# Kernel tuning notes

Hardware: AMD Instinct MI355X
Metric: run time of the kernel (lower is better)

Reference implementation:

```python
import jax, jax.numpy as jnp
import numpy as np

B, N, C = 4, 2048, 1024
H = 16
D = C // H
FF = 4096
EPS = 1e-6


def _layernorm(x, g, b):
    mu = jnp.mean(x, axis=-1, keepdims=True)
    var = jnp.mean(jnp.square(x - mu), axis=-1, keepdims=True)
    return (x - mu) * jax.lax.rsqrt(var + EPS) * g + b


def setup_inputs() -> dict:
    key = jax.random.key(0)
    ks = jax.random.split(key, 8)
    s = 0.02
    x = jax.random.normal(ks[0], (B, N, C), dtype=jnp.float32)
    mask = jnp.tril(jnp.ones((N, N), dtype=bool))[None, None]  # causal [1,1,N,N]
    return {
        "x": x,
        "mask": mask,
        "qkv_w": jax.random.normal(ks[1], (3 * C, C), jnp.float32) * s,
        "qkv_b": jnp.zeros((3 * C,), jnp.float32),
        "proj_w": jax.random.normal(ks[2], (C, C), jnp.float32) * s,
        "proj_b": jnp.zeros((C,), jnp.float32),
        "ln1_g": jnp.ones((C,), jnp.float32),
        "ln1_b": jnp.zeros((C,), jnp.float32),
        "ln2_g": jnp.ones((C,), jnp.float32),
        "ln2_b": jnp.zeros((C,), jnp.float32),
        "w1": jax.random.normal(ks[3], (FF, C), jnp.float32) * s,
        "w2": jax.random.normal(ks[4], (C, FF), jnp.float32) * s,
        "w3": jax.random.normal(ks[5], (FF, C), jnp.float32) * s,
    }


def reference(x, mask, qkv_w, qkv_b, proj_w, proj_b, ln1_g, ln1_b, ln2_g, ln2_b, w1, w2, w3):
    # --- attention sub-block (pre-norm) ---
    h = _layernorm(x, ln1_g, ln1_b)
    qkv = h @ qkv_w.T + qkv_b                      # [B,N,3C]
    qkv = qkv.reshape(B, N, 3, H, D).transpose(2, 0, 3, 1, 4)  # [3,B,H,N,D]
    q, k, v = qkv[0], qkv[1], qkv[2]
    scale = D ** -0.5
    attn = jnp.einsum("bhnd,bhmd->bhnm", q, k) * scale
    attn = jnp.where(mask, attn, -jnp.inf)
    attn = jax.nn.softmax(attn, axis=-1)
    o = jnp.einsum("bhnm,bhmd->bhnd", attn, v)
    o = o.transpose(0, 2, 1, 3).reshape(B, N, C)
    o = o @ proj_w.T + proj_b
    x = x + o  # dropout is identity in eval mode
    # --- SwiGLU MLP sub-block (pre-norm) ---
    h = _layernorm(x, ln2_g, ln2_b)
    m = (jax.nn.silu(h @ w1.T) * (h @ w3.T)) @ w2.T
    return x + m
```

## Files before the change

### kernel.cpp

```cpp
#include <hip/hip_runtime.h>
#include <hip/hip_bf16.h>
#include <stdint.h>

#define NB   4
#define NSEQ 2048
#define NC   1024
#define NH   16
#define ND   64
#define NFF  4096
#define NM   (NB*NSEQ)

typedef __attribute__((ext_vector_type(8))) short short8v;
typedef __attribute__((ext_vector_type(4))) short short4v;
typedef __attribute__((ext_vector_type(4))) float f32x4;

#define GPTR(p) ((const __attribute__((address_space(1))) void*)(p))
#define LPTR(p) ((__attribute__((address_space(3))) void*)(p))

__device__ __forceinline__ short f2bf(float f){
  unsigned u = __builtin_bit_cast(unsigned, f);
  u += 0x7fffu + ((u >> 16) & 1u);
  return (short)(u >> 16);
}
__device__ __forceinline__ float bf2f(short h){
  unsigned u = ((unsigned)(unsigned short)h) << 16;
  return __builtin_bit_cast(float, u);
}
__device__ __forceinline__ f32x4 mfma16x32(short8v a, short8v b, f32x4 c){
  return __builtin_amdgcn_mfma_f32_16x16x32_bf16(a, b, c, 0, 0, 0);
}
__device__ __forceinline__ f32x4 mfma16x16(short4v a, short4v b, f32x4 c){
  return __builtin_amdgcn_mfma_f32_16x16x16bf16_1k(a, b, c, 0, 0, 0);
}
__device__ __forceinline__ short4v pack4bf(f32x4 v){
  __hip_bfloat162 a = __float22bfloat162_rn(float2{v[0], v[1]});
  __hip_bfloat162 b = __float22bfloat162_rn(float2{v[2], v[3]});
  short4v r;
  __builtin_memcpy(&r, &a, 4);
  __builtin_memcpy(((char*)&r) + 4, &b, 4);
  return r;
}

__global__ __launch_bounds__(256) void cvt_kernel(const float* __restrict__ w,
                                                  short* __restrict__ o, int n){
  int i = (blockIdx.x * 256 + threadIdx.x) * 4;
  if (i >= n) return;
  float4 v = *(const float4*)(w + i);
  short4v r = { f2bf(v.x), f2bf(v.y), f2bf(v.z), f2bf(v.w) };
  *(short4v*)(o + i) = r;
}

__global__ __launch_bounds__(256) void ln_kernel(const float* __restrict__ x,
                                                 const float* __restrict__ g,
                                                 const float* __restrict__ bta,
                                                 short* __restrict__ out){
  int row = blockIdx.x;
  int tid = threadIdx.x;
  int lane = tid & 63, w = tid >> 6;
  const float4* xr = (const float4*)(x + (size_t)row * NC);
  float4 v = xr[tid];
  float s1 = v.x + v.y + v.z + v.w;
  float s2 = v.x*v.x + v.y*v.y + v.z*v.z + v.w*v.w;
  #pragma unroll
  for (int off = 32; off; off >>= 1){
    s1 += __shfl_xor(s1, off);
    s2 += __shfl_xor(s2, off);
  }
  __shared__ float red[8];
  if (lane == 0){ red[w] = s1; red[4 + w] = s2; }
  __syncthreads();
  s1 = red[0] + red[1] + red[2] + red[3];
  s2 = red[4] + red[5] + red[6] + red[7];
  float mean = s1 * (1.0f / NC);
  float var  = s2 * (1.0f / NC) - mean * mean;
  float inv  = rsqrtf(var + 1e-6f);
  float4 gv = ((const float4*)g)[tid];
  float4 bv = ((const float4*)bta)[tid];
  short4v o = { f2bf((v.x - mean) * inv * gv.x + bv.x),
                f2bf((v.y - mean) * inv * gv.y + bv.y),
                f2bf((v.z - mean) * inv * gv.z + bv.z),
                f2bf((v.w - mean) * inv * gv.w + bv.w) };
  *(short4v*)(out + (size_t)row * NC + tid * 4) = o;
}

template<bool HAS_BIAS, bool HAS_RES, bool OUT_BF16, bool QKV_V>
__global__ __launch_bounds__(256, 3) void gemm_bt(const short* __restrict__ A,
                                                  const short* __restrict__ Bm,
                                                  const float* __restrict__ bias,
                                                  const float* __restrict__ res,
                                                  void* __restrict__ outp,
                                                  short* __restrict__ vt,
                                                  int Nc, int K){
  __shared__ short Al[128 * 64];
  __shared__ short Bl[128 * 64];
  int tid = threadIdx.x;
  int gx = gridDim.x, nwg = gx * gridDim.y;
  int wg = blockIdx.y * gx + blockIdx.x;
  int swz = (wg & 7) * (nwg >> 3) + (wg >> 3);
  int m0 = (swz / gx) * 128, n0 = (swz % gx) * 128;
  const short* Ag = A + (size_t)m0 * K;
  const short* Bg = Bm + (size_t)n0 * K;
  int lane = tid & 63, wid = tid >> 6;
  int wm = (wid >> 1) * 64, wn = (wid & 1) * 64;
  int qd = lane >> 4, l15 = lane & 15;

  f32x4 acc[4][4] = {};

  for (int k0 = 0; k0 < K; k0 += 64){
    __syncthreads();
    #pragma unroll
    for (int i = 0; i < 4; i++){
      int cg = (wid * 4 + i) * 64 + lane;
      int r  = cg >> 3, c = cg & 7;
      int sc = (c ^ (r & 7)) << 3;
      __builtin_amdgcn_global_load_lds(GPTR(Ag + (size_t)r * K + k0 + sc),
                                       LPTR(&Al[cg * 8]), 16, 0, 0);
      __builtin_amdgcn_global_load_lds(GPTR(Bg + (size_t)r * K + k0 + sc),
                                       LPTR(&Bl[cg * 8]), 16, 0, 0);
    }
    __syncthreads();
    #pragma unroll
    for (int kk = 0; kk < 2; kk++){
      short8v a[4], b[4];
      #pragma unroll
      for (int t = 0; t < 4; t++){
        int r = wm + t * 16 + l15;
        a[t] = *(const short8v*)&Al[r * 64 + (((kk * 4 + qd) ^ (r & 7)) << 3)];
      }
      #pragma unroll
      for (int t = 0; t < 4; t++){
        int r = wn + t * 16 + l15;
        b[t] = *(const short8v*)&Bl[r * 64 + (((kk * 4 + qd) ^ (r & 7)) << 3)];
      }
      #pragma unroll
      for (int i = 0; i < 4; i++)
        #pragma unroll
        for (int j = 0; j < 4; j++)
          acc[i][j] = mfma16x32(a[i], b[j], acc[i][j]);
    }
  }

  #pragma unroll
  for (int ti = 0; ti < 4; ti++){
    #pragma unroll
    for (int tj = 0; tj < 4; tj++){
      int col = n0 + wn + tj * 16 + l15;
      float bv = HAS_BIAS ? bias[col] : 0.0f;
      #pragma unroll
      for (int r = 0; r < 4; r++){
        int row = m0 + wm + ti * 16 + qd * 4 + r;
        float v = acc[ti][tj][r] + bv;
        if (QKV_V && col >= 2048){
          int hh = (col - 2048) >> 6, dd = col & 63;
          int bb = row >> 11, nn = row & 2047;
          vt[(((size_t)(bb * 16 + hh) * 64 + dd) << 11) + nn] = f2bf(v);
        } else {
          size_t idx = (size_t)row * Nc + col;
          if (HAS_RES) v += res[idx];
          if (OUT_BF16) ((short*)outp)[idx] = f2bf(v);
          else          ((float*)outp)[idx] = v;
        }
      }
    }
  }
}

__global__ __launch_bounds__(256, 2) void gemm_ff13(const short* __restrict__ A,
                                                    const short* __restrict__ B1m,
                                                    const short* __restrict__ B3m,
                                                    short* __restrict__ outp){
  __shared__ short Al [128 * 64];
  __shared__ short B1l[128 * 64];
  __shared__ short B3l[128 * 64];
  int tid = threadIdx.x;
  int gx = gridDim.x;
  int wg = blockIdx.y * gx + blockIdx.x;
  int xcd = wg & 7, idx = wg >> 3;
  int npx = gx >> 3;
  int n0 = (xcd * npx + idx % npx) * 128;
  int m0 = (idx / npx) * 128;
  const short* Ag  = A   + (size_t)m0 * NC;
  const short* B1g = B1m + (size_t)n0 * NC;
  const short* B3g = B3m + (size_t)n0 * NC;
  int lane = tid & 63, wid = tid >> 6;
  int wm = (wid >> 1) * 64, wn = (wid & 1) * 64;
  int qd = lane >> 4, l15 = lane & 15;

  f32x4 acc1[4][4] = {}, acc3[4][4] = {};

  for (int k0 = 0; k0 < NC; k0 += 64){
    __syncthreads();
    #pragma unroll
    for (int i = 0; i < 4; i++){
      int cg = (wid * 4 + i) * 64 + lane;
      int r  = cg >> 3, c = cg & 7;
      int sc = (c ^ (r & 7)) << 3;
      __builtin_amdgcn_global_load_lds(GPTR(Ag + (size_t)r * NC + k0 + sc),
                                       LPTR(&Al[cg * 8]), 16, 0, 0);
      __builtin_amdgcn_global_load_lds(GPTR(B1g + (size_t)r * NC + k0 + sc),
                                       LPTR(&B1l[cg * 8]), 16, 0, 0);
      __builtin_amdgcn_global_load_lds(GPTR(B3g + (size_t)r * NC + k0 + sc),
                                       LPTR(&B3l[cg * 8]), 16, 0, 0);
    }
    __syncthreads();
    #pragma unroll
    for (int kk = 0; kk < 2; kk++){
      short8v a[4], b1[4], b3[4];
      #pragma unroll
      for (int t = 0; t < 4; t++){
        int r = wm + t * 16 + l15;
        a[t] = *(const short8v*)&Al[r * 64 + (((kk * 4 + qd) ^ (r & 7)) << 3)];
      }
      #pragma unroll
      for (int t = 0; t < 4; t++){
        int r = wn + t * 16 + l15;
        int co = ((kk * 4 + qd) ^ (r & 7)) << 3;
        b1[t] = *(const short8v*)&B1l[r * 64 + co];
        b3[t] = *(const short8v*)&B3l[r * 64 + co];
      }
      #pragma unroll
      for (int i = 0; i < 4; i++)
        #pragma unroll
        for (int j = 0; j < 4; j++){
          acc1[i][j] = mfma16x32(a[i], b1[j], acc1[i][j]);
          acc3[i][j] = mfma16x32(a[i], b3[j], acc3[i][j]);
        }
    }
  }

  #pragma unroll
  for (int ti = 0; ti < 4; ti++){
    #pragma unroll
    for (int tj = 0; tj < 4; tj++){
      int col = n0 + wn + tj * 16 + l15;
      #pragma unroll
      for (int r = 0; r < 4; r++){
        int row = m0 + wm + ti * 16 + qd * 4 + r;
        float v1 = acc1[ti][tj][r];
        float v3 = acc3[ti][tj][r];
        float s = v1 / (1.0f + __expf(-v1)) * v3;
        outp[(size_t)row * NFF + col] = f2bf(s);
      }
    }
  }
}

__global__ __launch_bounds__(256) void attn_kernel(const short* __restrict__ qkvb,
                                                   const short* __restrict__ vt,
                                                   short* __restrict__ outb){
  const float QSCALE = 0.125f * 1.44269504f;
  int bh = blockIdx.x;
  int qb = 15 - blockIdx.y;
  int b = bh >> 4, h = bh & 15;
  int tid = threadIdx.x;
  int lane = tid & 63, wid = tid >> 6;
  int qd = lane >> 4, l15 = lane & 15;
  int qs = qb * 128 + wid * 32;

  const short* qbase = qkvb + (size_t)b * NSEQ * 3072 + h * 64;
  const short* kbase = qbase + 1024;
  const short* vtb   = vt + ((size_t)bh << 17);

  __shared__ short Kl[2][64 * 64];
  __shared__ short Vl[2][64 * 64];

  short8v qf[2][2];
  #pragma unroll
  for (int g = 0; g < 2; g++)
    #pragma unroll
    for (int kc = 0; kc < 2; kc++){
      short8v q = *(const short8v*)(qbase + (size_t)(qs + g * 16 + l15) * 3072
                                    + kc * 32 + qd * 8);
      short8v r;
      #pragma unroll
      for (int j = 0; j < 8; j++) r[j] = f2bf(bf2f(q[j]) * QSCALE);
      qf[g][kc] = r;
    }

  float l_i[2] = { 0.f, 0.f };
  f32x4 o[2][4];
  #pragma unroll
  for (int g = 0; g < 2; g++)
    #pragma unroll
    for (int t = 0; t < 4; t++)
      o[g][t] = (f32x4){0.f, 0.f, 0.f, 0.f};

  int nkt_blk = 2 * qb + 2;
  int itmax   = (qs + 31) >> 6;

  auto STAGE = [&](int bufi, int k0){
    #pragma unroll
    for (int i = 0; i < 2; i++){
      int cg = (wid * 2 + i) * 64 + lane;
      int r  = cg >> 3, c = cg & 7;
      int sc = (c ^ (r & 7)) << 3;
      __builtin_amdgcn_global_load_lds(GPTR(kbase + (size_t)(k0 + r) * 3072 + sc),
                                       LPTR(&Kl[bufi][cg * 8]), 16, 0, 0);
      __builtin_amdgcn_global_load_lds(GPTR(vtb + ((size_t)r << 11) + k0 + sc),
                                       LPTR(&Vl[bufi][cg * 8]), 16, 0, 0);
    }
  };

  STAGE(0, 0);
  __syncthreads();
  int cur = 0;

  for (int it = 0; it < nkt_blk; ++it){
    if (it + 1 < nkt_blk) STAGE(cur ^ 1, (it + 1) * 64);

    if (it <= itmax){
      int k0 = it * 64;
      short8v kf[4][2];
      #pragma unroll
      for (int kt = 0; kt < 4; kt++)
        #pragma unroll
        for (int kc = 0; kc < 2; kc++){
          int r = kt * 16 + l15;
          kf[kt][kc] = *(const short8v*)
              &Kl[cur][r * 64 + (((kc * 4 + qd) ^ (r & 7)) << 3)];
        }
      short4v vf[4][4];
      #pragma unroll
      for (int t = 0; t < 4; t++)
        #pragma unroll
        for (int ks = 0; ks < 4; ks++){
          int r = t * 16 + l15;
          vf[t][ks] = *(const short4v*)
              &Vl[cur][r * 64 + (((ks * 2 + (qd >> 1)) ^ (r & 7)) << 3)
                       + ((qd & 1) << 2)];
        }

      f32x4 s[2][4];
      #pragma unroll
      for (int g = 0; g < 2; g++)
        #pragma unroll
        for (int kt = 0; kt < 4; kt++){
          f32x4 z = (f32x4){0.f, 0.f, 0.f, 0.f};
          z = mfma16x32(kf[kt][0], qf[g][0], z);
          s[g][kt] = mfma16x32(kf[kt][1], qf[g][1], z);
        }

      if (it == itmax){
        #pragma unroll
        for (int g = 0; g < 2; g++){
          int qg = qs + g * 16 + l15;
          #pragma unroll
          for (int kt = 0; kt < 4; kt++)
            #pragma unroll
            for (int r = 0; r < 4; r++){
              int kg = k0 + kt * 16 + qd * 4 + r;
              s[g][kt][r] = (kg <= qg) ? s[g][kt][r] : -1e30f;
            }
        }
      }

      short4v pb[2][4];
      #pragma unroll
      for (int g = 0; g < 2; g++){
        #pragma unroll
        for (int kt = 0; kt < 4; kt++){
          f32x4 p;
          #pragma unroll
          for (int r = 0; r < 4; r++){
            float pv = exp2f(fminf(s[g][kt][r], 24.0f));
            p[r] = pv;
            l_i[g] += pv;
          }
          pb[g][kt] = pack4bf(p);
        }
      }

      #pragma unroll
      for (int g = 0; g < 2; g++)
        #pragma unroll
        for (int t = 0; t < 4; t++)
          #pragma unroll
          for (int ks = 0; ks < 4; ks++)
            o[g][t] = mfma16x16(vf[t][ks], pb[g][ks], o[g][t]);
    }

    __syncthreads();
    cur ^= 1;
  }

  #pragma unroll
  for (int g = 0; g < 2; g++){
    float l = l_i[g];
    l += __shfl_xor(l, 16);
    l += __shfl_xor(l, 32);
    float inv_l = 1.0f / l;
    int q = qs + g * 16 + l15;
    size_t rowbase = ((size_t)(b * NSEQ + q)) * NC + h * 64;
    #pragma unroll
    for (int t = 0; t < 4; t++){
      f32x4 v = { o[g][t][0] * inv_l, o[g][t][1] * inv_l,
                  o[g][t][2] * inv_l, o[g][t][3] * inv_l };
      *(short4v*)(outb + rowbase + t * 16 + qd * 4) = pack4bf(v);
    }
  }
}

extern "C" void kernel_launch(void* const* d_in, const int* in_sizes, int n_in,
                              void* d_out, int out_size, void* d_ws, size_t ws_size,
                              hipStream_t stream){
  const float* x      = (const float*)d_in[0];
  const float* qkv_w  = (const float*)d_in[2];
  const float* qkv_b  = (const float*)d_in[3];
  const float* proj_w = (const float*)d_in[4];
  const float* proj_b = (const float*)d_in[5];
  const float* ln1_g  = (const float*)d_in[6];
  const float* ln1_b  = (const float*)d_in[7];
  const float* ln2_g  = (const float*)d_in[8];
  const float* ln2_b  = (const float*)d_in[9];
  const float* w1     = (const float*)d_in[10];
  const float* w2     = (const float*)d_in[11];
  const float* w3     = (const float*)d_in[12];
  float* out = (float*)d_out;

  short* wqkv  = (short*)d_ws;
  short* wproj = wqkv  + (size_t)3072 * 1024;
  short* w1b   = wproj + (size_t)1024 * 1024;
  short* w3b   = w1b   + (size_t)4096 * 1024;
  short* w2b   = w3b   + (size_t)4096 * 1024;
  short* hb    = w2b   + (size_t)4096 * 1024;
  short* qkvb  = hb    + (size_t)NM * NC;
  short* attnb = qkvb  + (size_t)NM * 3072;
  short* ff3b  = attnb + (size_t)NM * NC;
  float* x1    = (float*)(ff3b + (size_t)NM * NFF);
  short* ff1b  = qkvb;
  short* vtb   = ff3b;

  cvt_kernel<<<3072 * 1024 / 1024, 256, 0, stream>>>(qkv_w, wqkv, 3072 * 1024);
  cvt_kernel<<<1024, 256, 0, stream>>>(proj_w, wproj, 1024 * 1024);
  cvt_kernel<<<4096, 256, 0, stream>>>(w1, w1b, 4096 * 1024);
  cvt_kernel<<<4096, 256, 0, stream>>>(w3, w3b, 4096 * 1024);
  cvt_kernel<<<4096, 256, 0, stream>>>(w2, w2b, 4096 * 1024);

  ln_kernel<<<NM, 256, 0, stream>>>(x, ln1_g, ln1_b, hb);
  gemm_bt<true, false, true, true><<<dim3(3072 / 128, NM / 128), 256, 0, stream>>>(
      hb, wqkv, qkv_b, nullptr, qkvb, vtb, 3072, 1024);
  attn_kernel<<<dim3(NB * NH, NSEQ / 128), 256, 0, stream>>>(qkvb, vtb, attnb);
  gemm_bt<true, true, false, false><<<dim3(1024 / 128, NM / 128), 256, 0, stream>>>(
      attnb, wproj, proj_b, x, x1, nullptr, 1024, 1024);
  ln_kernel<<<NM, 256, 0, stream>>>(x1, ln2_g, ln2_b, hb);
  gemm_ff13<<<dim3(4096 / 128, NM / 128), 256, 0, stream>>>(hb, w1b, w3b, ff1b);
  gemm_bt<false, true, false, false><<<dim3(1024 / 128, NM / 128), 256, 0, stream>>>(
      ff1b, w2b, nullptr, x1, out, nullptr, 1024, 4096);
}
```

Baseline: 554.1 us.

## Pipeline GEMMs with triple-buffered LDS and 256x128 tiles on 8 waves

Replaces the synchronous load-then-compute GEMM loops with a three-stage LDS ring. Tiles for k-step t+2 are prefetched via global_load_lds while MFMAs run on step t, with explicit vmcnt waits and raw barriers instead of __syncthreads. Workgroups grow to 512 threads covering 256x128 output tiles, and the FF13 kernel switches to a 32-wide K step with a new swizzle. This aims to hide global-load latency and raise data reuse per tile, at the cost of more LDS per block, lower occupancy and fragile hand-counted waitcnt logic.

```diff
diff --git a/kernel.cpp b/kernel.cpp
--- a/kernel.cpp
+++ b/kernel.cpp
@@ -84,60 +84,92 @@
 }
 
 template<bool HAS_BIAS, bool HAS_RES, bool OUT_BF16, bool QKV_V>
-__global__ __launch_bounds__(256, 3) void gemm_bt(const short* __restrict__ A,
-                                                  const short* __restrict__ Bm,
-                                                  const float* __restrict__ bias,
-                                                  const float* __restrict__ res,
-                                                  void* __restrict__ outp,
-                                                  short* __restrict__ vt,
-                                                  int Nc, int K){
-  __shared__ short Al[128 * 64];
-  __shared__ short Bl[128 * 64];
+__global__ __launch_bounds__(512) void gemm8p(const short* __restrict__ A,
+                                              const short* __restrict__ Bm,
+                                              const float* __restrict__ bias,
+                                              const float* __restrict__ res,
+                                              void* __restrict__ outp,
+                                              short* __restrict__ vt,
+                                              int Nc, int K){
+  __shared__ short lds[3][(256 + 128) * 64];
   int tid = threadIdx.x;
   int gx = gridDim.x, nwg = gx * gridDim.y;
   int wg = blockIdx.y * gx + blockIdx.x;
   int swz = (wg & 7) * (nwg >> 3) + (wg >> 3);
-  int m0 = (swz / gx) * 128, n0 = (swz % gx) * 128;
+  int m0 = (swz / gx) * 256, n0 = (swz % gx) * 128;
   const short* Ag = A + (size_t)m0 * K;
   const short* Bg = Bm + (size_t)n0 * K;
   int lane = tid & 63, wid = tid >> 6;
   int wm = (wid >> 1) * 64, wn = (wid & 1) * 64;
   int qd = lane >> 4, l15 = lane & 15;
 
+  auto STAGE_A = [&](short* buf, const short* src, int i){
+    int cg = i * 512 + tid;
+    int r = cg >> 3, c = cg & 7;
+    __builtin_amdgcn_global_load_lds(GPTR(src + (size_t)r * K + ((c ^ (r & 7)) << 3)),
+                                     LPTR(buf + cg * 8), 16, 0, 0);
+  };
+  auto STAGE_B = [&](short* buf, const short* src, int i){
+    int cg = i * 512 + tid;
+    int r = cg >> 3, c = cg & 7;
+    __builtin_amdgcn_global_load_lds(GPTR(src + (size_t)r * K + ((c ^ (r & 7)) << 3)),
+                                     LPTR(buf + 256 * 64 + cg * 8), 16, 0, 0);
+  };
+
+  short* b0 = &lds[0][0];
+  short* b1 = &lds[1][0];
+  short* b2 = &lds[2][0];
+
+  int nt = K >> 6;
+  #pragma unroll
+  for (int i = 0; i < 4; i++) STAGE_A(b0, Ag, i);
+  #pragma unroll
+  for (int i = 0; i < 2; i++) STAGE_B(b0, Bg, i);
+  #pragma unroll
+  for (int i = 0; i < 4; i++) STAGE_A(b1, Ag + 64, i);
+  #pragma unroll
+  for (int i = 0; i < 2; i++) STAGE_B(b1, Bg + 64, i);
+  asm volatile("s_waitcnt vmcnt(6)" ::: "memory");
+  __builtin_amdgcn_s_barrier();
+
   f32x4 acc[4][4] = {};
 
-  for (int k0 = 0; k0 < K; k0 += 64){
-    __syncthreads();
-    #pragma unroll
-    for (int i = 0; i < 4; i++){
-      int cg = (wid * 4 + i) * 64 + lane;
-      int r  = cg >> 3, c = cg & 7;
-      int sc = (c ^ (r & 7)) << 3;
-      __builtin_amdgcn_global_load_lds(GPTR(Ag + (size_t)r * K + k0 + sc),
-                                       LPTR(&Al[cg * 8]), 16, 0, 0);
-      __builtin_amdgcn_global_load_lds(GPTR(Bg + (size_t)r * K + k0 + sc),
-                                       LPTR(&Bl[cg * 8]), 16, 0, 0);
-    }
-    __syncthreads();
-    #pragma unroll
-    for (int kk = 0; kk < 2; kk++){
+  for (int t = 0; t < nt; ++t){
+    bool pf = (t + 2) < nt;
+    const short* As = Ag + (size_t)(t + 2) * 64;
+    const short* Bs = Bg + (size_t)(t + 2) * 64;
+    #pragma unroll
+    for (int p = 0; p < 2; p++){
       short8v a[4], b[4];
       #pragma unroll
-      for (int t = 0; t < 4; t++){
-        int r = wm + t * 16 + l15;
-        a[t] = *(const short8v*)&Al[r * 64 + (((kk * 4 + qd) ^ (r & 7)) << 3)];
-      }
-      #pragma unroll
-      for (int t = 0; t < 4; t++){
-        int r = wn + t * 16 + l15;
-        b[t] = *(const short8v*)&Bl[r * 64 + (((kk * 4 + qd) ^ (r & 7)) << 3)];
-      }
+      for (int u = 0; u < 4; u++){
+        int r = wm + u * 16 + l15;
+        a[u] = *(const short8v*)&b0[r * 64 + (((p * 4 + qd) ^ (r & 7)) << 3)];
+      }
+      #pragma unroll
+      for (int u = 0; u < 4; u++){
+        int r = wn + u * 16 + l15;
+        b[u] = *(const short8v*)&b0[256 * 64 + r * 64 + (((p * 4 + qd) ^ (r & 7)) << 3)];
+      }
+      if (pf){
+        if (p == 0){ STAGE_A(b2, As, 0); STAGE_A(b2, As, 1); STAGE_B(b2, Bs, 0); }
+        else       { STAGE_A(b2, As, 2); STAGE_A(b2, As, 3); STAGE_B(b2, Bs, 1); }
+      }
+      __builtin_amdgcn_s_barrier();
+      __builtin_amdgcn_s_setprio(1);
       #pragma unroll
       for (int i = 0; i < 4; i++)
         #pragma unroll
         for (int j = 0; j < 4; j++)
           acc[i][j] = mfma16x32(a[i], b[j], acc[i][j]);
-    }
+      __builtin_amdgcn_s_setprio(0);
+      if (p == 1){
+        if (pf)                asm volatile("s_waitcnt vmcnt(6)" ::: "memory");
+        else if (t + 1 < nt)   asm volatile("s_waitcnt vmcnt(0)" ::: "memory");
+      }
+      __builtin_amdgcn_s_barrier();
+    }
+    short* tmp = b0; b0 = b1; b1 = b2; b2 = tmp;
   }
 
   #pragma unroll
@@ -165,20 +197,19 @@
   }
 }
 
-__global__ __launch_bounds__(256, 2) void gemm_ff13(const short* __restrict__ A,
-                                                    const short* __restrict__ B1m,
-                                                    const short* __restrict__ B3m,
-                                                    short* __restrict__ outp){
-  __shared__ short Al [128 * 64];
-  __shared__ short B1l[128 * 64];
-  __shared__ short B3l[128 * 64];
+__global__ __launch_bounds__(512) void gemm_ff13(const short* __restrict__ A,
+                                                 const short* __restrict__ B1m,
+                                                 const short* __restrict__ B3m,
+                                                 short* __restrict__ outp){
+  __shared__ short lds[3][(256 + 128 + 128) * 32];
+  const int AOFF = 256 * 32, B3OFF = 256 * 32 + 128 * 32;
   int tid = threadIdx.x;
   int gx = gridDim.x;
   int wg = blockIdx.y * gx + blockIdx.x;
   int xcd = wg & 7, idx = wg >> 3;
   int npx = gx >> 3;
   int n0 = (xcd * npx + idx % npx) * 128;
-  int m0 = (idx / npx) * 128;
+  int m0 = (idx / npx) * 256;
   const short* Ag  = A   + (size_t)m0 * NC;
   const short* B1g = B1m + (size_t)n0 * NC;
   const short* B3g = B3m + (size_t)n0 * NC;
@@ -186,46 +217,68 @@
   int wm = (wid >> 1) * 64, wn = (wid & 1) * 64;
   int qd = lane >> 4, l15 = lane & 15;
 
+  auto STAGE_A = [&](short* buf, const short* src, int i){
+    int cg = i * 512 + tid;
+    int r = cg >> 2, c = cg & 3;
+    __builtin_amdgcn_global_load_lds(GPTR(src + (size_t)r * NC + ((c ^ ((r >> 1) & 3)) << 3)),
+                                     LPTR(buf + cg * 8), 16, 0, 0);
+  };
+  auto STAGE_Bx = [&](short* buf, const short* src, int off){
+    int cg = tid;
+    int r = cg >> 2, c = cg & 3;
+    __builtin_amdgcn_global_load_lds(GPTR(src + (size_t)r * NC + ((c ^ ((r >> 1) & 3)) << 3)),
+                                     LPTR(buf + off + cg * 8), 16, 0, 0);
+  };
+
+  short* b0 = &lds[0][0];
+  short* b1 = &lds[1][0];
+  short* b2 = &lds[2][0];
+
+  STAGE_A(b0, Ag, 0); STAGE_A(b0, Ag, 1);
+  STAGE_Bx(b0, B1g, AOFF); STAGE_Bx(b0, B3g, B3OFF);
+  STAGE_A(b1, Ag + 32, 0); STAGE_A(b1, Ag + 32, 1);
+  STAGE_Bx(b1, B1g + 32, AOFF); STAGE_Bx(b1, B3g + 32, B3OFF);
+  asm volatile("s_waitcnt vmcnt(4)" ::: "memory");
+  __builtin_amdgcn_s_barrier();
+
   f32x4 acc1[4][4] = {}, acc3[4][4] = {};
 
-  for (int k0 = 0; k0 < NC; k0 += 64){
-    __syncthreads();
-    #pragma unroll
-    for (int i = 0; i < 4; i++){
-      int cg = (wid * 4 + i) * 64 + lane;
-      int r  = cg >> 3, c = cg & 7;
-      int sc = (c ^ (r & 7)) << 3;
-      __builtin_amdgcn_global_load_lds(GPTR(Ag + (size_t)r * NC + k0 + sc),
-                                       LPTR(&Al[cg * 8]), 16, 0, 0);
-      __builtin_amdgcn_global_load_lds(GPTR(B1g + (size_t)r * NC + k0 + sc),
-                                       LPTR(&B1l[cg * 8]), 16, 0, 0);
-      __builtin_amdgcn_global_load_lds(GPTR(B3g + (size_t)r * NC + k0 + sc),
-                                       LPTR(&B3l[cg * 8]), 16, 0, 0);
-    }
-    __syncthreads();
-    #pragma unroll
-    for (int kk = 0; kk < 2; kk++){
-      short8v a[4], b1[4], b3[4];
-      #pragma unroll
-      for (int t = 0; t < 4; t++){
-        int r = wm + t * 16 + l15;
-        a[t] = *(const short8v*)&Al[r * 64 + (((kk * 4 + qd) ^ (r & 7)) << 3)];
-      }
-      #pragma unroll
-      for (int t = 0; t < 4; t++){
-        int r = wn + t * 16 + l15;
-        int co = ((kk * 4 + qd) ^ (r & 7)) << 3;
-        b1[t] = *(const short8v*)&B1l[r * 64 + co];
-        b3[t] = *(const short8v*)&B3l[r * 64 + co];
-      }
-      #pragma unroll
-      for (int i = 0; i < 4; i++)
-        #pragma unroll
-        for (int j = 0; j < 4; j++){
-          acc1[i][j] = mfma16x32(a[i], b1[j], acc1[i][j]);
-          acc3[i][j] = mfma16x32(a[i], b3[j], acc3[i][j]);
-        }
-    }
+  const int nt = NC / 32;
+  for (int t = 0; t < nt; ++t){
+    bool pf = (t + 2) < nt;
+    const short* As = Ag + (size_t)(t + 2) * 32;
+    short8v a[4], c1[4], c3[4];
+    #pragma unroll
+    for (int u = 0; u < 4; u++){
+      int r = wm + u * 16 + l15;
+      a[u] = *(const short8v*)&b0[r * 32 + ((qd ^ ((r >> 1) & 3)) << 3)];
+    }
+    #pragma unroll
+    for (int u = 0; u < 4; u++){
+      int r = wn + u * 16 + l15;
+      int co = (qd ^ ((r >> 1) & 3)) << 3;
+      c1[u] = *(const short8v*)&b0[AOFF  + r * 32 + co];
+      c3[u] = *(const short8v*)&b0[B3OFF + r * 32 + co];
+    }
+    if (pf){
+      STAGE_A(b2, As, 0); STAGE_A(b2, As, 1);
+      STAGE_Bx(b2, B1g + (size_t)(t + 2) * 32, AOFF);
+      STAGE_Bx(b2, B3g + (size_t)(t + 2) * 32, B3OFF);
+    }
+    __builtin_amdgcn_s_barrier();
+    __builtin_amdgcn_s_setprio(1);
+    #pragma unroll
+    for (int i = 0; i < 4; i++)
+      #pragma unroll
+      for (int j = 0; j < 4; j++){
+        acc1[i][j] = mfma16x32(a[i], c1[j], acc1[i][j]);
+        acc3[i][j] = mfma16x32(a[i], c3[j], acc3[i][j]);
+      }
+    __builtin_amdgcn_s_setprio(0);
+    if (pf)              asm volatile("s_waitcnt vmcnt(4)" ::: "memory");
+    else if (t + 1 < nt) asm volatile("s_waitcnt vmcnt(0)" ::: "memory");
+    __builtin_amdgcn_s_barrier();
+    short* tmp = b0; b0 = b1; b1 = b2; b2 = tmp;
   }
 
   #pragma unroll
@@ -437,13 +490,13 @@
   cvt_kernel<<<4096, 256, 0, stream>>>(w2, w2b, 4096 * 1024);
 
   ln_kernel<<<NM, 256, 0, stream>>>(x, ln1_g, ln1_b, hb);
-  gemm_bt<true, false, true, true><<<dim3(3072 / 128, NM / 128), 256, 0, stream>>>(
+  gemm8p<true, false, true, true><<<dim3(3072 / 128, NM / 256), 512, 0, stream>>>(
       hb, wqkv, qkv_b, nullptr, qkvb, vtb, 3072, 1024);
   attn_kernel<<<dim3(NB * NH, NSEQ / 128), 256, 0, stream>>>(qkvb, vtb, attnb);
-  gemm_bt<true, true, false, false><<<dim3(1024 / 128, NM / 128), 256, 0, stream>>>(
+  gemm8p<true, true, false, false><<<dim3(1024 / 128, NM / 256), 512, 0, stream>>>(
       attnb, wproj, proj_b, x, x1, nullptr, 1024, 1024);
   ln_kernel<<<NM, 256, 0, stream>>>(x1, ln2_g, ln2_b, hb);
-  gemm_ff13<<<dim3(4096 / 128, NM / 128), 256, 0, stream>>>(hb, w1b, w3b, ff1b);
-  gemm_bt<false, true, false, false><<<dim3(1024 / 128, NM / 128), 256, 0, stream>>>(
+  gemm_ff13<<<dim3(4096 / 128, NM / 256), 512, 0, stream>>>(hb, w1b, w3b, ff1b);
+  gemm8p<false, true, false, false><<<dim3(1024 / 128, NM / 256), 512, 0, stream>>>(
       ff1b, w2b, nullptr, x1, out, nullptr, 1024, 4096);
 }
```

Result: slower. 574.6 us (+3.7%).
